# Performance work log

Measured on AMD Instinct MI355X. Metric: run time of the kernel, lower is better.

The kernel has to match this reference:

```python
import jax, jax.numpy as jnp
import numpy as np

BN_EPS = 1e-5


def setup_inputs() -> dict:
    key = jax.random.key(0)
    ks = jax.random.split(key, 8)
    b, c, h, w, d = 16, 256, 128, 128, 64
    x = jax.random.normal(ks[0], (b, c, h, w), dtype=jnp.float32)
    conv1_w = jax.random.normal(ks[1], (c, c), dtype=jnp.float32) * np.sqrt(2.0 / c)
    conv1_b = jax.random.normal(ks[2], (c,), dtype=jnp.float32) * 0.02
    mk_w = jax.random.normal(ks[3], (d, c), dtype=jnp.float32) * np.sqrt(2.0 / d)
    mv_w = jnp.transpose(mk_w)  # original ties mv.weight = mk.weight.permute(1,0,2)
    conv2_w = jax.random.normal(ks[4], (c, c), dtype=jnp.float32) * np.sqrt(2.0 / c)
    bn_gamma = jnp.ones((c,), dtype=jnp.float32)
    bn_beta = jnp.zeros((c,), dtype=jnp.float32)
    bn_mean = jax.random.normal(ks[5], (c,), dtype=jnp.float32) * 0.1
    bn_var = jax.random.uniform(ks[6], (c,), dtype=jnp.float32, minval=0.5, maxval=1.5)
    return {"x": x, "conv1_w": conv1_w, "conv1_b": conv1_b, "mk_w": mk_w,
            "mv_w": mv_w, "conv2_w": conv2_w, "bn_gamma": bn_gamma,
            "bn_beta": bn_beta, "bn_mean": bn_mean, "bn_var": bn_var}


def reference(x, conv1_w, conv1_b, mk_w, mv_w, conv2_w, bn_gamma, bn_beta, bn_mean, bn_var):
    b, c, h, w = x.shape
    n = h * w
    identity = x
    # conv1: 1x1 conv with bias -> [b, c, n]
    y = jnp.einsum('oc,bchw->bohw', conv1_w, x) + conv1_b[None, :, None, None]
    y = y.reshape(b, c, n)
    # external attention: mk projection [b, d, n]
    attn = jnp.einsum('dc,bcn->bdn', mk_w, y)
    attn = jax.nn.softmax(attn, axis=-1)              # softmax over spatial N
    attn = attn / (1e-9 + attn.sum(axis=1, keepdims=True))  # column-normalize over d
    # mv projection back to channels [b, c, n]
    z = jnp.einsum('cd,bdn->bcn', mv_w, attn)
    z = z.reshape(b, c, h, w)
    # conv2 (1x1, no bias) + BatchNorm (inference) + residual + relu
    z = jnp.einsum('oc,bchw->bohw', conv2_w, z)
    inv = bn_gamma / jnp.sqrt(bn_var + BN_EPS)
    z = z * inv[None, :, None, None] + (bn_beta - bn_mean * inv)[None, :, None, None]
    return jax.nn.relu(z + identity)
```

## Files before the change

kernel.cpp:

```cpp
#include <hip/hip_runtime.h>
#include <hip/hip_bf16.h>

#define HW 16384
#define C  256
#define D  64
#define NB 16
#define M0 16.0f
#define LOG2E 1.44269504088896340736f

typedef unsigned short u16;
typedef __attribute__((ext_vector_type(4))) float  f32x4;
typedef __attribute__((ext_vector_type(4))) short  s16x4;
typedef __attribute__((ext_vector_type(8))) short  s16x8;

__device__ __forceinline__ float bf2f(u16 u) {
    return __uint_as_float(((unsigned int)u) << 16);
}
__device__ __forceinline__ short f2bfs(float f) {
    union { __hip_bfloat16 h; short s; } u;
    u.h = __float2bfloat16(f);
    return u.s;
}
__device__ __forceinline__ u16 f2bf(float f) {
    unsigned int u = __float_as_uint(f);
    unsigned int r = (u + 0x7fffu + ((u >> 16) & 1u)) >> 16;
    return (u16)r;
}

#define MFMA16(a, b, c) __builtin_amdgcn_mfma_f32_16x16x32_bf16((a), (b), (c), 0, 0, 0)

__global__ void precompute_kernel(const float* __restrict__ conv1_w,
                                  const float* __restrict__ conv1_b,
                                  const float* __restrict__ mk_w,
                                  const float* __restrict__ mv_w,
                                  const float* __restrict__ conv2_w,
                                  const float* __restrict__ gamma,
                                  const float* __restrict__ beta,
                                  const float* __restrict__ mean,
                                  const float* __restrict__ var,
                                  short* __restrict__ Ath,
                                  short* __restrict__ Atl,
                                  float* __restrict__ amk,
                                  short* __restrict__ Bmb,
                                  float* __restrict__ shift,
                                  float* __restrict__ esum)
{
    int gid = blockIdx.x * blockDim.x + threadIdx.x;
    if (gid < C * D) {
        int d = gid >> 8, cp = gid & 255;
        float s = 0.f;
        for (int c = 0; c < C; ++c) s += mk_w[d * C + c] * conv1_w[c * C + cp];
        u16 h = f2bf(s);
        Ath[gid] = (short)h;
        Atl[gid] = (short)f2bf(s - bf2f(h));
    } else if (gid < 2 * C * D) {
        int g = gid - C * D;
        int o = g >> 6, d = g & 63;
        float inv = gamma[o] * rsqrtf(var[o] + 1e-5f);
        float s = 0.f;
        for (int c = 0; c < C; ++c) s += conv2_w[o * C + c] * mv_w[c * D + d];
        Bmb[g] = (short)f2bf(s * inv);
    } else if (gid < 2 * C * D + D) {
        int d = gid - 2 * C * D;
        float s = 0.f;
        for (int c = 0; c < C; ++c) s += mk_w[d * C + c] * conv1_b[c];
        amk[d] = s;
    } else if (gid < 2 * C * D + D + C) {
        int o = gid - (2 * C * D + D);
        float inv = gamma[o] * rsqrtf(var[o] + 1e-5f);
        shift[o] = beta[o] - mean[o] * inv;
    } else if (gid < 2 * C * D + D + C + NB * D) {
        esum[gid - (2 * C * D + D + C)] = 0.f;
    }
}

#define NT1 64
#define CH  128
#define XR1 (CH + 8)
__global__ __launch_bounds__(256, 5) void pexp_kernel(const float* __restrict__ x,
                                                      const short* __restrict__ Ath,
                                                      const short* __restrict__ Atl,
                                                      const float* __restrict__ amk,
                                                      short* __restrict__ xb16,
                                                      u16* __restrict__ pexp,
                                                      float* __restrict__ esum)
{
    __shared__ short xs[NT1 * XR1];
    const int t = threadIdx.x;
    const int b = blockIdx.y;
    const int n0 = blockIdx.x * NT1;
    const int lane = t & 63, w = t >> 6;
    const int col = lane & 15, g = lane >> 4;

    const float* xb = x + (size_t)b * C * HW + n0;
    short* xg = xb16 + (size_t)b * C * HW + n0;

    f32x4 zz = {0.f, 0.f, 0.f, 0.f};
    f32x4 acc[4] = { zz, zz, zz, zz };

    for (int h = 0; h < 2; ++h) {
        const int ch = h * CH;
        if (h) __syncthreads();

        #pragma unroll
        for (int i = 0; i < 2; ++i) {
            int cell = i * 256 + t;
            int nq = cell & 15, cq = cell >> 4;
            int c0 = cq * 4, nn = nq * 4;
            const float* gp = xb + (size_t)(ch + c0) * HW + nn;
            f32x4 r0 = __builtin_nontemporal_load((const f32x4*)(gp));
            f32x4 r1 = __builtin_nontemporal_load((const f32x4*)(gp + HW));
            f32x4 r2 = __builtin_nontemporal_load((const f32x4*)(gp + 2 * HW));
            f32x4 r3 = __builtin_nontemporal_load((const f32x4*)(gp + 3 * HW));
            short v[4][4];
            #pragma unroll
            for (int j = 0; j < 4; ++j) {
                v[0][j] = f2bfs(r0[j]); v[1][j] = f2bfs(r1[j]);
                v[2][j] = f2bfs(r2[j]); v[3][j] = f2bfs(r3[j]);
            }
            #pragma unroll
            for (int j = 0; j < 4; ++j) {
                s16x4 hi = { v[0][j], v[1][j], v[2][j], v[3][j] };
                *(s16x4*)&xs[(nn + j) * XR1 + c0] = hi;
            }
            #pragma unroll
            for (int r = 0; r < 4; ++r) {
                s16x4 vr = { v[r][0], v[r][1], v[r][2], v[r][3] };
                *(s16x4*)(xg + (size_t)(ch + c0 + r) * HW + nn) = vr;
            }
        }

        s16x8 Ah[4], Al[4];
        {
            const short* ah = Ath + (size_t)(w * 16 + col) * C + ch + 8 * g;
            const short* al = Atl + (size_t)(w * 16 + col) * C + ch + 8 * g;
            #pragma unroll
            for (int ks = 0; ks < 4; ++ks) {
                Ah[ks] = *(const s16x8*)(ah + ks * 32);
                Al[ks] = *(const s16x8*)(al + ks * 32);
            }
        }
        __syncthreads();

        #pragma unroll
        for (int ks = 0; ks < 4; ++ks) {
            #pragma unroll
            for (int nt = 0; nt < 4; ++nt) {
                s16x8 xf = *(const s16x8*)&xs[(nt * 16 + col) * XR1 + ks * 32 + 8 * g];
                acc[nt] = MFMA16(xf, Ah[ks], acc[nt]);
                acc[nt] = MFMA16(xf, Al[ks], acc[nt]);
            }
        }
    }

    const float am = amk[w * 16 + col];
    u16* pb = pexp + (size_t)b * D * HW + (size_t)(w * 16 + col) * HW + n0;
    float rs = 0.f;
    #pragma unroll
    for (int nt = 0; nt < 4; ++nt) {
        s16x4 st4;
        #pragma unroll
        for (int r = 0; r < 4; ++r) {
            float e = exp2f((acc[nt][r] + am - M0) * LOG2E);
            rs += e;
            st4[r] = f2bfs(e);
        }
        *(s16x4*)(pb + nt * 16 + 4 * g) = st4;
    }
    rs += __shfl_xor(rs, 16);
    rs += __shfl_xor(rs, 32);
    if (lane < 16) atomicAdd(esum + b * D + w * 16 + lane, rs);
}

#define NT3 64
__global__ __launch_bounds__(256, 3) void out_kernel(const short* __restrict__ xb16,
                                                     const u16* __restrict__ pexp,
                                                     const float* __restrict__ esum,
                                                     const short* __restrict__ Bmb,
                                                     const float* __restrict__ shift,
                                                     float* __restrict__ out)
{
    __shared__ short ps[NT3 * 72];
    __shared__ float csum[4][NT3];
    __shared__ float rr[NT3];

    const int t = threadIdx.x;
    const int b  = (NB - 1) - blockIdx.y;
    const int n0 = ((int)gridDim.x - 1 - blockIdx.x) * NT3;

    {
        const int nl = t & 63, dq = t >> 6;
        const u16* lg = pexp + (size_t)b * D * HW + (size_t)(dq * 16) * HW + n0 + nl;
        const float* es = esum + b * D + dq * 16;
        float cs = 0.f;
        #pragma unroll
        for (int j4 = 0; j4 < 4; ++j4) {
            s16x4 pk;
            #pragma unroll
            for (int jj = 0; jj < 4; ++jj) {
                int j = j4 * 4 + jj;
                float iv = __fdividef(1.0f, es[j]);
                float pv = bf2f(lg[(size_t)j * HW]) * iv;
                cs += pv;
                pk[jj] = f2bfs(pv);
            }
            *(s16x4*)&ps[nl * 72 + dq * 16 + j4 * 4] = pk;
        }
        csum[dq][nl] = cs;
    }
    __syncthreads();
    if (t < NT3)
        rr[t] = __fdividef(1.0f, csum[0][t] + csum[1][t] + csum[2][t] + csum[3][t] + 1e-9f);
    __syncthreads();

    const int lane = t & 63, col = lane & 15, g = lane >> 4;
    const int w = t >> 6;

    s16x8 Bf[4][2];
    #pragma unroll
    for (int ot = 0; ot < 4; ++ot) {
        const short* bp = Bmb + (size_t)(w * 64 + ot * 16 + col) * D + 8 * g;
        Bf[ot][0] = *(const s16x8*)(bp);
        Bf[ot][1] = *(const s16x8*)(bp + 32);
    }

    f32x4 zz = {0.f, 0.f, 0.f, 0.f};
    f32x4 acc[4][4];
    #pragma unroll
    for (int ot = 0; ot < 4; ++ot)
        #pragma unroll
        for (int nt = 0; nt < 4; ++nt) acc[ot][nt] = zz;

    #pragma unroll
    for (int nt = 0; nt < 4; ++nt) {
        const short* pr = &ps[(nt * 16 + col) * 72 + 8 * g];
        s16x8 p0 = *(const s16x8*)(pr);
        s16x8 p1 = *(const s16x8*)(pr + 32);
        #pragma unroll
        for (int ot = 0; ot < 4; ++ot) {
            acc[ot][nt] = MFMA16(p0, Bf[ot][0], acc[ot][nt]);
            acc[ot][nt] = MFMA16(p1, Bf[ot][1], acc[ot][nt]);
        }
    }

    float sh[4];
    #pragma unroll
    for (int ot = 0; ot < 4; ++ot) sh[ot] = shift[w * 64 + ot * 16 + col];

    const short* xh = xb16 + (size_t)b * C * HW + n0;
    float* ob = out + (size_t)b * C * HW + n0;
    #pragma unroll
    for (int nt = 0; nt < 4; ++nt) {
        f32x4 rv = *(const f32x4*)&rr[nt * 16 + 4 * g];
        #pragma unroll
        for (int ot = 0; ot < 4; ++ot) {
            const size_t off = (size_t)(w * 64 + ot * 16 + col) * HW + nt * 16 + 4 * g;
            s16x4 xq = *(const s16x4*)(xh + off);
            f32x4 vv;
            #pragma unroll
            for (int r = 0; r < 4; ++r)
                vv[r] = fmaxf(acc[ot][nt][r] * rv[r] + sh[ot] + bf2f((u16)xq[r]), 0.f);
            __builtin_nontemporal_store(vv, (f32x4*)(ob + off));
        }
    }
}

extern "C" void kernel_launch(void* const* d_in, const int* in_sizes, int n_in,
                              void* d_out, int out_size, void* d_ws, size_t ws_size,
                              hipStream_t stream)
{
    const float* x       = (const float*)d_in[0];
    const float* conv1_w = (const float*)d_in[1];
    const float* conv1_b = (const float*)d_in[2];
    const float* mk_w    = (const float*)d_in[3];
    const float* mv_w    = (const float*)d_in[4];
    const float* conv2_w = (const float*)d_in[5];
    const float* gamma   = (const float*)d_in[6];
    const float* beta    = (const float*)d_in[7];
    const float* mean    = (const float*)d_in[8];
    const float* var     = (const float*)d_in[9];
    float* out = (float*)d_out;

    float* amk   = (float*)d_ws;
    float* shift = amk + D;
    float* esum  = shift + C;
    short* Ath   = (short*)(esum + NB * D);
    short* Atl   = Ath + C * D;
    short* Bmb   = Atl + C * D;
    short* xb16  = Bmb + C * D;
    u16* pexp    = (u16*)(xb16 + (size_t)NB * C * HW);

    const int pre_work = 2 * C * D + D + C + NB * D;
    precompute_kernel<<<(pre_work + 255) / 256, 256, 0, stream>>>(
        conv1_w, conv1_b, mk_w, mv_w, conv2_w, gamma, beta, mean, var,
        Ath, Atl, amk, Bmb, shift, esum);

    pexp_kernel<<<dim3(HW / NT1, NB), 256, 0, stream>>>(x, Ath, Atl, amk,
                                                        xb16, pexp, esum);

    out_kernel<<<dim3(HW / NT3, NB), 256, 0, stream>>>(xb16, pexp, esum,
                                                       Bmb, shift, out);
}
```

Baseline: 533.0 us.

## Stage pexp and output tiles through LDS for coalesced global writes

The pexp kernel now writes its bf16 exp tile into shared memory and then stores it to global memory as full 16-byte row segments, replacing the scattered 8-byte stores. The output kernel processes output channels in four chunks of 64. Each chunk's MFMA accumulators go through a padded LDS buffer so that every row of 64 outputs is written with contiguous float4 stores, and the residual is read the same way. This targets poorly coalesced global stores and lowers register pressure (launch bounds raised to 4 blocks per CU). The cost is extra LDS traffic and more __syncthreads per chunk.

```diff
diff --git a/kernel.cpp b/kernel.cpp
--- a/kernel.cpp
+++ b/kernel.cpp
@@ -77,6 +77,7 @@
 #define NT1 64
 #define CH  128
 #define XR1 (CH + 8)
+#define PB  72
 __global__ __launch_bounds__(256, 5) void pexp_kernel(const float* __restrict__ x,
                                                       const short* __restrict__ Ath,
                                                       const short* __restrict__ Atl,
@@ -86,6 +87,7 @@
                                                       float* __restrict__ esum)
 {
     __shared__ short xs[NT1 * XR1];
+    __shared__ short pbuf[D * PB];
     const int t = threadIdx.x;
     const int b = blockIdx.y;
     const int n0 = blockIdx.x * NT1;
@@ -154,7 +156,6 @@
     }
 
     const float am = amk[w * 16 + col];
-    u16* pb = pexp + (size_t)b * D * HW + (size_t)(w * 16 + col) * HW + n0;
     float rs = 0.f;
     #pragma unroll
     for (int nt = 0; nt < 4; ++nt) {
@@ -165,22 +166,37 @@
             rs += e;
             st4[r] = f2bfs(e);
         }
-        *(s16x4*)(pb + nt * 16 + 4 * g) = st4;
+        *(s16x4*)&pbuf[(w * 16 + col) * PB + nt * 16 + 4 * g] = st4;
     }
     rs += __shfl_xor(rs, 16);
     rs += __shfl_xor(rs, 32);
     if (lane < 16) atomicAdd(esum + b * D + w * 16 + lane, rs);
+    __syncthreads();
+
+    {
+        const int seg = t & 7, row8 = t >> 3;
+        u16* pB = pexp + (size_t)b * D * HW + n0;
+        #pragma unroll
+        for (int p = 0; p < 2; ++p) {
+            const int d = p * 32 + row8;
+            s16x8 v8 = *(const s16x8*)&pbuf[d * PB + seg * 8];
+            *(s16x8*)(pB + (size_t)d * HW + seg * 8) = v8;
+        }
+    }
 }
 
 #define NT3 64
-__global__ __launch_bounds__(256, 3) void out_kernel(const short* __restrict__ xb16,
+#define PR3 72
+#define OBS 68
+__global__ __launch_bounds__(256, 4) void out_kernel(const short* __restrict__ xb16,
                                                      const u16* __restrict__ pexp,
                                                      const float* __restrict__ esum,
                                                      const short* __restrict__ Bmb,
                                                      const float* __restrict__ shift,
                                                      float* __restrict__ out)
 {
-    __shared__ short ps[NT3 * 72];
+    __shared__ short ps[NT3 * PR3];
+    __shared__ float obuf[64 * OBS];
     __shared__ float csum[4][NT3];
     __shared__ float rr[NT3];
 
@@ -204,7 +220,7 @@
                 cs += pv;
                 pk[jj] = f2bfs(pv);
             }
-            *(s16x4*)&ps[nl * 72 + dq * 16 + j4 * 4] = pk;
+            *(s16x4*)&ps[nl * PR3 + dq * 16 + j4 * 4] = pk;
         }
         csum[dq][nl] = cs;
     }
@@ -216,51 +232,47 @@
     const int lane = t & 63, col = lane & 15, g = lane >> 4;
     const int w = t >> 6;
 
-    s16x8 Bf[4][2];
-    #pragma unroll
-    for (int ot = 0; ot < 4; ++ot) {
-        const short* bp = Bmb + (size_t)(w * 64 + ot * 16 + col) * D + 8 * g;
-        Bf[ot][0] = *(const s16x8*)(bp);
-        Bf[ot][1] = *(const s16x8*)(bp + 32);
-    }
-
-    f32x4 zz = {0.f, 0.f, 0.f, 0.f};
-    f32x4 acc[4][4];
-    #pragma unroll
-    for (int ot = 0; ot < 4; ++ot)
-        #pragma unroll
-        for (int nt = 0; nt < 4; ++nt) acc[ot][nt] = zz;
-
-    #pragma unroll
-    for (int nt = 0; nt < 4; ++nt) {
-        const short* pr = &ps[(nt * 16 + col) * 72 + 8 * g];
-        s16x8 p0 = *(const s16x8*)(pr);
-        s16x8 p1 = *(const s16x8*)(pr + 32);
-        #pragma unroll
-        for (int ot = 0; ot < 4; ++ot) {
-            acc[ot][nt] = MFMA16(p0, Bf[ot][0], acc[ot][nt]);
-            acc[ot][nt] = MFMA16(p1, Bf[ot][1], acc[ot][nt]);
-        }
-    }
-
-    float sh[4];
-    #pragma unroll
-    for (int ot = 0; ot < 4; ++ot) sh[ot] = shift[w * 64 + ot * 16 + col];
-
     const short* xh = xb16 + (size_t)b * C * HW + n0;
     float* ob = out + (size_t)b * C * HW + n0;
-    #pragma unroll
-    for (int nt = 0; nt < 4; ++nt) {
-        f32x4 rv = *(const f32x4*)&rr[nt * 16 + 4 * g];
-        #pragma unroll
-        for (int ot = 0; ot < 4; ++ot) {
-            const size_t off = (size_t)(w * 64 + ot * 16 + col) * HW + nt * 16 + 4 * g;
-            s16x4 xq = *(const s16x4*)(xh + off);
+
+    for (int chunk = 0; chunk < 4; ++chunk) {
+        const int ob0 = chunk * 64 + w * 16;
+
+        const short* bp = Bmb + (size_t)(ob0 + col) * D + 8 * g;
+        s16x8 B0 = *(const s16x8*)(bp);
+        s16x8 B1 = *(const s16x8*)(bp + 32);
+
+        f32x4 zz = {0.f, 0.f, 0.f, 0.f};
+        f32x4 acc[4] = { zz, zz, zz, zz };
+        #pragma unroll
+        for (int nt = 0; nt < 4; ++nt) {
+            const short* pr = &ps[(nt * 16 + col) * PR3 + 8 * g];
+            s16x8 p0 = *(const s16x8*)(pr);
+            s16x8 p1 = *(const s16x8*)(pr + 32);
+            acc[nt] = MFMA16(p0, B0, acc[nt]);
+            acc[nt] = MFMA16(p1, B1, acc[nt]);
+        }
+
+        if (chunk) __syncthreads();
+        #pragma unroll
+        for (int nt = 0; nt < 4; ++nt)
+            *(f32x4*)&obuf[(w * 16 + col) * OBS + nt * 16 + 4 * g] = acc[nt];
+        __syncthreads();
+
+        const int seg = t & 15, row16 = t >> 4;
+        #pragma unroll
+        for (int p = 0; p < 4; ++p) {
+            const int row = p * 16 + row16;
+            const int o = chunk * 64 + row;
+            f32x4 a  = *(const f32x4*)&obuf[row * OBS + seg * 4];
+            f32x4 rv = *(const f32x4*)&rr[seg * 4];
+            const float sh = shift[o];
+            s16x4 xq = *(const s16x4*)(xh + (size_t)o * HW + seg * 4);
             f32x4 vv;
             #pragma unroll
             for (int r = 0; r < 4; ++r)
-                vv[r] = fmaxf(acc[ot][nt][r] * rv[r] + sh[ot] + bf2f((u16)xq[r]), 0.f);
-            __builtin_nontemporal_store(vv, (f32x4*)(ob + off));
+                vv[r] = fmaxf(a[r] * rv[r] + sh + bf2f((u16)xq[r]), 0.f);
+            __builtin_nontemporal_store(vv, (f32x4*)(ob + (size_t)o * HW + seg * 4));
         }
     }
 }
```

New measurement: 514.4 us. -3.5%, faster.
